# Performance work log

Hardware: AMD Instinct MI355X
Metric: run time of the kernel (lower is better)

The kernel has to match this reference:

```python
import jax, jax.numpy as jnp
import numpy as np

N, L, D = 4096, 16, 768        # nodes, max name tokens, gpt2 embed dim
NH_NAME = 4                    # name-encoder attention heads
H, NH, NL, C = 1024, 8, 4, 16  # hidden, encoder heads, encoder layers, classes
XF = 256                       # raw node feature dim; feat_dim = XF + D = 1024
VOCAB = 50257


def _ln(x, g, b, eps=1e-5):
    m = jnp.mean(x, axis=-1, keepdims=True)
    v = jnp.var(x, axis=-1, keepdims=True)
    return (x - m) * jax.lax.rsqrt(v + eps) * g + b


def _mha(x, in_w, in_b, out_w, out_b, nh, key_mask=None):
    # x: [B, S, E]; in_w: [3E, E] (torch nn.MultiheadAttention packed qkv)
    B, S, E = x.shape
    dh = E // nh
    qkv = x @ in_w.T + in_b
    q, k, v = jnp.split(qkv, 3, axis=-1)
    q = q.reshape(B, S, nh, dh)
    k = k.reshape(B, S, nh, dh)
    v = v.reshape(B, S, nh, dh)
    scores = jnp.einsum('bqhd,bkhd->bhqk', q, k) / jnp.sqrt(jnp.asarray(dh, x.dtype))
    if key_mask is not None:
        scores = jnp.where(key_mask[:, None, None, :], scores, jnp.asarray(-1e9, x.dtype))
    a = jax.nn.softmax(scores, axis=-1)
    o = jnp.einsum('bhqk,bkhd->bqhd', a, v).reshape(B, S, E)
    return o @ out_w.T + out_b


def setup_inputs() -> dict:
    key = jax.random.key(0)
    ks = jax.random.split(key, 16)
    s = 0.02
    r = lambda i, shape: jax.random.normal(ks[i], shape, jnp.float32) * s
    return {
        'name_tokens': jax.random.randint(ks[0], (N, L), 0, VOCAB),
        'name_lens': jax.random.randint(ks[1], (N,), 1, L + 1),
        'x_feats': jax.random.normal(ks[2], (N, XF), jnp.float32),
        'wte': r(3, (VOCAB, D)),
        'mha_in_w': r(4, (3 * D, D)), 'mha_in_b': jnp.zeros((3 * D,), jnp.float32),
        'mha_out_w': r(5, (D, D)), 'mha_out_b': jnp.zeros((D,), jnp.float32),
        'bott_w': r(6, (H, XF + D)), 'bott_b': jnp.zeros((H,), jnp.float32),
        'enc_in_w': r(7, (NL, 3 * H, H)), 'enc_in_b': jnp.zeros((NL, 3 * H), jnp.float32),
        'enc_out_w': r(8, (NL, H, H)), 'enc_out_b': jnp.zeros((NL, H), jnp.float32),
        'enc_ln1_g': jnp.ones((NL, H), jnp.float32), 'enc_ln1_b': jnp.zeros((NL, H), jnp.float32),
        'enc_ln2_g': jnp.ones((NL, H), jnp.float32), 'enc_ln2_b': jnp.zeros((NL, H), jnp.float32),
        'enc_ff1_w': r(9, (NL, 2 * H, H)), 'enc_ff1_b': jnp.zeros((NL, 2 * H), jnp.float32),
        'enc_ff2_w': r(10, (NL, H, 2 * H)), 'enc_ff2_b': jnp.zeros((NL, H), jnp.float32),
        'cls_w': r(11, (C, H)), 'cls_b': jnp.zeros((C,), jnp.float32),
    }


def reference(name_tokens, name_lens, x_feats, wte,
              mha_in_w, mha_in_b, mha_out_w, mha_out_b,
              bott_w, bott_b,
              enc_in_w, enc_in_b, enc_out_w, enc_out_b,
              enc_ln1_g, enc_ln1_b, enc_ln2_g, enc_ln2_b,
              enc_ff1_w, enc_ff1_b, enc_ff2_w, enc_ff2_b,
              cls_w, cls_b):
    # --- GraphNameEncoder: batched over all N ragged name sequences ---
    mask = jnp.arange(L)[None, :] < name_lens[:, None]          # [N, L] valid-token mask
    emb = wte[name_tokens]                                      # [N, L, D]
    attn = _mha(emb, mha_in_w, mha_in_b, mha_out_w, mha_out_b, NH_NAME, key_mask=mask)
    name_emb = jnp.sum(jnp.where(mask[:, :, None], attn, 0.0), axis=1)  # [N, D]
    x = jnp.concatenate([x_feats, name_emb], axis=-1)           # [N, XF + D]
    # --- bottleneck ---
    x = x @ bott_w.T + bott_b                                   # [N, H]
    # --- TransformerEncoder on seq_len=1 (x.unsqueeze(1)), post-norm, relu ---
    h = x[:, None, :]                                           # [N, 1, H]
    for l in range(NL):
        a = _mha(h, enc_in_w[l], enc_in_b[l], enc_out_w[l], enc_out_b[l], NH)
        h = _ln(h + a, enc_ln1_g[l], enc_ln1_b[l])
        f = jax.nn.relu(h @ enc_ff1_w[l].T + enc_ff1_b[l]) @ enc_ff2_w[l].T + enc_ff2_b[l]
        h = _ln(h + f, enc_ln2_g[l], enc_ln2_b[l])
    out = h @ cls_w.T + cls_b                                   # [N, 1, C]
    return out[:, 0, :]                                         # squeeze -> [N, C]
```

## Files before the change

### kernel.cpp

```cpp
#include <hip/hip_runtime.h>

typedef unsigned short bf16_t;
typedef __attribute__((ext_vector_type(8))) __bf16 bf16x8;
typedef __attribute__((ext_vector_type(4))) float f32x4;

__device__ __forceinline__ float bf2f(unsigned v) { return __uint_as_float(v << 16); }
__device__ __forceinline__ bf16_t f2bf(float f) {
  unsigned u = __float_as_uint(f);
  return (bf16_t)((u + 0x7fffu + ((u >> 16) & 1u)) >> 16);
}
__device__ __forceinline__ unsigned pack2(float a, float b) {
  return (unsigned)f2bf(a) | ((unsigned)f2bf(b) << 16);
}

__global__ __launch_bounds__(256) void scan_lens(const int* __restrict__ lens,
                                                 int* __restrict__ offs,
                                                 int* __restrict__ Mact) {
  __shared__ int wsum[4];
  const int t = threadIdx.x;
  int v[16]; int s = 0;
#pragma unroll
  for (int i = 0; i < 16; i++) { v[i] = lens[t * 16 + i]; s += v[i]; }
  const int lane = t & 63, w = t >> 6;
  int x = s;
#pragma unroll
  for (int o = 1; o < 64; o <<= 1) {
    int y = __shfl_up(x, o);
    if (lane >= o) x += y;
  }
  if (lane == 63) wsum[w] = x;
  __syncthreads();
  int base = 0;
  for (int i = 0; i < w; i++) base += wsum[i];
  int run = base + x - s;
#pragma unroll
  for (int i = 0; i < 16; i++) { offs[t * 16 + i] = run; run += v[i]; }
  if (t == 255) Mact[0] = run;
}

__global__ void cvt_f32_bf16(const float* __restrict__ src, bf16_t* __restrict__ dst, long n4) {
  long i = (long)blockIdx.x * blockDim.x + threadIdx.x;
  if (i >= n4) return;
  float4 v = ((const float4*)src)[i];
  ((uint2*)dst)[i] = make_uint2(pack2(v.x, v.y), pack2(v.z, v.w));
}

__global__ __launch_bounds__(256) void cvt_trans(const float* __restrict__ src,
                                                 bf16_t* __restrict__ dst) {
  __shared__ float tile[32][33];
  const int l = blockIdx.z;
  const int bx = blockIdx.x * 32;
  const int by = blockIdx.y * 32;
  const float* s = src + (size_t)l * 3 * 1024 * 1024 + 2 * 1024 * 1024;
  const int tx = threadIdx.x & 31, ty = threadIdx.x >> 5;
#pragma unroll
  for (int i = 0; i < 32; i += 8)
    tile[ty + i][tx] = s[(size_t)(by + ty + i) * 1024 + bx + tx];
  __syncthreads();
  bf16_t* d = dst + (size_t)l * 1024 * 1024;
#pragma unroll
  for (int i = 0; i < 32; i += 8)
    d[(size_t)(bx + ty + i) * 1024 + by + tx] = f2bf(tile[tx][ty + i]);
}

__global__ __launch_bounds__(256) void bias_comb(const float* __restrict__ enc_out_w,
                                                 const float* __restrict__ enc_in_b,
                                                 const float* __restrict__ enc_out_b,
                                                 float* __restrict__ bc) {
  const int l = blockIdx.y;
  const int wave = threadIdx.x >> 6, lane = threadIdx.x & 63;
  const float* w = enc_out_w + (size_t)l * 1024 * 1024;
  const float* bv = enc_in_b + (size_t)l * 3072 + 2048;
  for (int c = wave; c < 16; c += 4) {
    int i = blockIdx.x * 16 + c;
    const float* wr = w + (size_t)i * 1024;
    float acc = 0.f;
    for (int j = lane; j < 1024; j += 64) acc += wr[j] * bv[j];
#pragma unroll
    for (int o = 32; o > 0; o >>= 1) acc += __shfl_down(acc, o);
    if (lane == 0) bc[(size_t)l * 1024 + i] = acc + enc_out_b[(size_t)l * 1024 + i];
  }
}

__global__ void gather_emb_c(const int* __restrict__ tok, const int* __restrict__ lens,
                             const int* __restrict__ offs, const float* __restrict__ wte,
                             bf16_t* __restrict__ emb) {
  long i = (long)blockIdx.x * blockDim.x + threadIdx.x;
  if (i >= 65536L * 192L) return;
  long nl = i / 192; int cg = (int)(i % 192);
  int n = (int)(nl >> 4), l = (int)(nl & 15);
  if (l >= lens[n]) return;
  long ro = (long)offs[n] + l;
  int t = tok[nl];
  float4 v = *(const float4*)(wte + (long)t * 768 + cg * 4);
  ((uint2*)emb)[ro * 192 + cg] = make_uint2(pack2(v.x, v.y), pack2(v.z, v.w));
}

__global__ void xfeat_lenf(const float* __restrict__ xf, const int* __restrict__ lens,
                           bf16_t* __restrict__ x, float* __restrict__ lenf) {
  long i = (long)blockIdx.x * blockDim.x + threadIdx.x;
  if (i < 4096) lenf[i] = (float)lens[i];
  if (i >= 4096L * 64L) return;
  int row = (int)(i >> 6); int c4 = (int)(i & 63) * 4;
  float4 v = *(const float4*)(xf + (long)row * 256 + c4);
  *(uint2*)(x + (long)row * 1024 + c4) = make_uint2(pack2(v.x, v.y), pack2(v.z, v.w));
}

#define BM 128
#define BN 128
#define BK 32
#define SBT (BM * BK + BN * BK)

__device__ __forceinline__ void async16(const void* g, void* l) {
  __builtin_amdgcn_global_load_lds((const __attribute__((address_space(1))) void*)g,
                                   (__attribute__((address_space(3))) void*)l, 16, 0, 0);
}

__global__ __launch_bounds__(256, 2) void gemm_bt(
    const bf16_t* __restrict__ A, const bf16_t* __restrict__ W,
    const float* __restrict__ bias, bf16_t* __restrict__ C,
    int K, int ldc, const int* __restrict__ Mp,
    long sA, long sB, long sC) {
  const int m0 = blockIdx.y * BM;
  if (Mp != nullptr && m0 >= *Mp) return;
  __shared__ __attribute__((aligned(16))) bf16_t smem[2 * SBT];
  const int t = threadIdx.x;
  const int n0 = blockIdx.x * BN;
  const int z = blockIdx.z;
  const int lane = t & 63;
  const int wr = t >> 7;
  const int wc = (t >> 6) & 1;
  const int quad = lane >> 4;
  const int r16 = lane & 15;

  f32x4 acc[4][4] = {};

  const int c0 = t, c1 = t + 256;
  const int row0 = c0 >> 2, kp0 = (c0 & 3) << 3;
  const int row1 = c1 >> 2, kp1 = (c1 & 3) << 3;
  const size_t oc0 = (size_t)(c0 & ~63) * 8;
  const size_t oc1 = (size_t)(c1 & ~63) * 8;
  const bf16_t* Ab = A + (size_t)z * sA + (size_t)m0 * K;
  const bf16_t* Wb = W + (size_t)z * sB + (size_t)n0 * K;
  bf16_t* Cb = C + (size_t)z * sC;

  auto stage = [&](int b, int k0) {
    bf16_t* As = smem + (size_t)b * SBT;
    bf16_t* Bs = As + BM * BK;
    async16(Ab + (size_t)row0 * K + k0 + kp0, As + oc0);
    async16(Ab + (size_t)row1 * K + k0 + kp1, As + oc1);
    async16(Wb + (size_t)row0 * K + k0 + kp0, Bs + oc0);
    async16(Wb + (size_t)row1 * K + k0 + kp1, Bs + oc1);
  };

  stage(0, 0);
  __syncthreads();
  int cur = 0;
  for (int k0 = 0; k0 < K; k0 += BK) {
    if (k0 + BK < K) stage(cur ^ 1, k0 + BK);
    const bf16_t* As = smem + (size_t)cur * SBT;
    const bf16_t* Bs = As + BM * BK;
    bf16x8 af[4], bfr[4];
#pragma unroll
    for (int i = 0; i < 4; i++) {
      af[i]  = *(const bf16x8*)(As + (wr * 64 + i * 16 + r16) * BK + quad * 8);
      bfr[i] = *(const bf16x8*)(Bs + (wc * 64 + i * 16 + r16) * BK + quad * 8);
    }
#pragma unroll
    for (int i = 0; i < 4; i++)
#pragma unroll
      for (int j = 0; j < 4; j++)
        acc[i][j] = __builtin_amdgcn_mfma_f32_16x16x32_bf16(af[i], bfr[j], acc[i][j], 0, 0, 0);
    __syncthreads();
    cur ^= 1;
  }

  const int ldcs = 136;
  bf16_t* Cs = smem;
#pragma unroll
  for (int s = 0; s < 4; s++) {
    if (wr == (s >> 1)) {
      const int ib = (s & 1) * 2;
#pragma unroll
      for (int i2 = 0; i2 < 2; i2++) {
        const int i = ib + i2;
#pragma unroll
        for (int j = 0; j < 4; j++) {
          int col = wc * 64 + j * 16 + r16;
          float bv = bias ? bias[n0 + col] : 0.0f;
#pragma unroll
          for (int r = 0; r < 4; r++)
            Cs[(i2 * 16 + quad * 4 + r) * ldcs + col] = f2bf(acc[i][j][r] + bv);
        }
      }
    }
    __syncthreads();
    {
      const int rl = t >> 4, cl = (t & 15) * 8;
#pragma unroll
      for (int p = 0; p < 2; p++) {
        int row = rl + p * 16;
        bf16x8 v = *(const bf16x8*)(Cs + row * ldcs + cl);
        *(bf16x8*)(Cb + (size_t)(m0 + s * 32 + row) * ldc + n0 + cl) = v;
      }
    }
    __syncthreads();
  }
}

#define S64 (128 * 64 + 64 * 64)

template <bool RELU>
__global__ __launch_bounds__(256, 3) void gemm128x64(
    const bf16_t* __restrict__ A, const bf16_t* __restrict__ W,
    const float* __restrict__ bias, const float* __restrict__ rowscale,
    bf16_t* __restrict__ C, int K, int ldc) {
  __shared__ __attribute__((aligned(16))) bf16_t smem[2 * S64];
  const int t = threadIdx.x;
  const int m0 = blockIdx.x * 128, n0 = blockIdx.y * 64;
  const int lane = t & 63, w = t >> 6;
  const int quad = lane >> 4, r16 = lane & 15;
  f32x4 acc[2][4] = {};
  int rowA[4], kpA[4];
  size_t oA[4];
#pragma unroll
  for (int i = 0; i < 4; i++) {
    int c = t + i * 256;
    rowA[i] = c >> 3;
    kpA[i] = ((c & 7) ^ (rowA[i] & 7)) << 3;
    oA[i] = (size_t)(c & ~63) * 8;
  }
  int rowB[2], kpB[2];
  size_t oB[2];
#pragma unroll
  for (int i = 0; i < 2; i++) {
    int c = t + i * 256;
    rowB[i] = c >> 3;
    kpB[i] = ((c & 7) ^ (rowB[i] & 7)) << 3;
    oB[i] = (size_t)(c & ~63) * 8;
  }
  const bf16_t* Ab = A + (size_t)m0 * K;
  const bf16_t* Wb = W + (size_t)n0 * K;

  auto stage = [&](int b, int k0) {
    bf16_t* As = smem + (size_t)b * S64;
    bf16_t* Bs = As + 128 * 64;
#pragma unroll
    for (int i = 0; i < 4; i++) async16(Ab + (size_t)rowA[i] * K + k0 + kpA[i], As + oA[i]);
#pragma unroll
    for (int i = 0; i < 2; i++) async16(Wb + (size_t)rowB[i] * K + k0 + kpB[i], Bs + oB[i]);
  };

  stage(0, 0);
  __syncthreads();
  int cur = 0;
  for (int k0 = 0; k0 < K; k0 += 64) {
    if (k0 + 64 < K) stage(cur ^ 1, k0 + 64);
    const bf16_t* As = smem + (size_t)cur * S64;
    const bf16_t* Bs = As + 128 * 64;
#pragma unroll
    for (int kk8 = 0; kk8 < 8; kk8 += 4) {
      bf16x8 af[2], bfr[4];
#pragma unroll
      for (int i = 0; i < 2; i++) {
        int Ra = w * 32 + i * 16 + r16;
        af[i] = *(const bf16x8*)(As + Ra * 64 + (((kk8 + quad) ^ (Ra & 7)) << 3));
      }
#pragma unroll
      for (int j = 0; j < 4; j++) {
        int Rb = j * 16 + r16;
        bfr[j] = *(const bf16x8*)(Bs + Rb * 64 + (((kk8 + quad) ^ (Rb & 7)) << 3));
      }
#pragma unroll
      for (int i = 0; i < 2; i++)
#pragma unroll
        for (int j = 0; j < 4; j++)
          acc[i][j] = __builtin_amdgcn_mfma_f32_16x16x32_bf16(af[i], bfr[j], acc[i][j], 0, 0, 0);
    }
    __syncthreads();
    cur ^= 1;
  }

  const int ldcs = 72;
  bf16_t* Cs = smem;
#pragma unroll
  for (int i = 0; i < 2; i++) {
#pragma unroll
    for (int j = 0; j < 4; j++) {
      int col = j * 16 + r16;
      float bv = bias ? bias[n0 + col] : 0.0f;
#pragma unroll
      for (int r = 0; r < 4; r++) {
        int row = w * 32 + i * 16 + quad * 4 + r;
        float sc = rowscale ? rowscale[m0 + row] : 1.0f;
        float v = acc[i][j][r] + bv * sc;
        if (RELU) v = fmaxf(v, 0.0f);
        Cs[row * ldcs + col] = f2bf(v);
      }
    }
  }
  __syncthreads();
  {
    const int rl = t >> 3, cl = (t & 7) * 8;
#pragma unroll
    for (int p = 0; p < 4; p++) {
      int row = rl + p * 32;
      bf16x8 v = *(const bf16x8*)(Cs + row * ldcs + cl);
      *(bf16x8*)(C + (size_t)(m0 + row) * ldc + n0 + cl) = v;
    }
  }
}

__global__ __launch_bounds__(64) void attn_name(const bf16_t* __restrict__ qkv,
                                                const int* __restrict__ lens,
                                                const int* __restrict__ offs,
                                                bf16_t* __restrict__ s) {
  const int n = blockIdx.x, h = blockIdx.y;
  const int lane = threadIdx.x;
  __shared__ unsigned short qs[16][208];
  __shared__ unsigned short ks[16][208];
  __shared__ unsigned short vs[16][208];
  __shared__ float ps[16][16];
  __shared__ float wj[16];
  const int len = lens[n];
  const bf16_t* base = qkv + (size_t)offs[n] * 2304 + h * 192;
  for (int g = lane; g < len * 48; g += 64) {
    int row = g / 48, c4 = (g % 48) * 4;
    const bf16_t* p = base + (size_t)row * 2304 + c4;
    uint2 a;
    a = *(const uint2*)p;
    *(unsigned*)&qs[row][c4] = a.x; *(unsigned*)&qs[row][c4 + 2] = a.y;
    a = *(const uint2*)(p + 768);
    *(unsigned*)&ks[row][c4] = a.x; *(unsigned*)&ks[row][c4 + 2] = a.y;
    a = *(const uint2*)(p + 1536);
    *(unsigned*)&vs[row][c4] = a.x; *(unsigned*)&vs[row][c4 + 2] = a.y;
  }
  __syncthreads();
  {
    const int l = lane >> 2, j0 = (lane & 3) * 4;
    float s0 = 0, s1 = 0, s2 = 0, s3 = 0;
    for (int d = 0; d < 192; d++) {
      float q = bf2f(qs[l][d]);
      s0 += q * bf2f(ks[j0 + 0][d]);
      s1 += q * bf2f(ks[j0 + 1][d]);
      s2 += q * bf2f(ks[j0 + 2][d]);
      s3 += q * bf2f(ks[j0 + 3][d]);
    }
    const float sc = 0.07216878f;
    ps[l][j0 + 0] = s0 * sc; ps[l][j0 + 1] = s1 * sc;
    ps[l][j0 + 2] = s2 * sc; ps[l][j0 + 3] = s3 * sc;
  }
  __syncthreads();
  if (lane < 16) {
    float m = -1e30f;
    for (int j = 0; j < len; j++) m = fmaxf(m, ps[lane][j]);
    float sum = 0.f;
    for (int j = 0; j < len; j++) sum += __expf(ps[lane][j] - m);
    float inv = 1.0f / sum;
    for (int j = 0; j < 16; j++) ps[lane][j] = (j < len) ? __expf(ps[lane][j] - m) * inv : 0.0f;
  }
  __syncthreads();
  if (lane < 16) {
    float a = 0.f;
    for (int l2 = 0; l2 < len; l2++) a += ps[l2][lane];
    wj[lane] = a;
  }
  __syncthreads();
  for (int d = lane; d < 192; d += 64) {
    float a = 0.f;
    for (int j = 0; j < len; j++) a += wj[j] * bf2f(vs[j][d]);
    s[(size_t)n * 768 + h * 192 + d] = f2bf(a);
  }
}

__global__ __launch_bounds__(256) void ln_res(bf16_t* __restrict__ h, const bf16_t* __restrict__ d,
                                              const float* __restrict__ g, const float* __restrict__ b) {
  const int n = blockIdx.x, t = threadIdx.x;
  __shared__ float s1[4], s2[4];
  bf16_t* hr = h + (size_t)n * 1024;
  const bf16_t* dr = d + (size_t)n * 1024;
  float x[4];
  float sum = 0.f, ss = 0.f;
#pragma unroll
  for (int i = 0; i < 4; i++) {
    int c = t + i * 256;
    float v = bf2f(hr[c]) + bf2f(dr[c]);
    x[i] = v; sum += v; ss += v * v;
  }
#pragma unroll
  for (int o = 32; o > 0; o >>= 1) { sum += __shfl_down(sum, o); ss += __shfl_down(ss, o); }
  if ((t & 63) == 0) { s1[t >> 6] = sum; s2[t >> 6] = ss; }
  __syncthreads();
  sum = s1[0] + s1[1] + s1[2] + s1[3];
  ss  = s2[0] + s2[1] + s2[2] + s2[3];
  const float mean = sum * (1.0f / 1024.0f);
  const float var = ss * (1.0f / 1024.0f) - mean * mean;
  const float rstd = rsqrtf(var + 1e-5f);
#pragma unroll
  for (int i = 0; i < 4; i++) {
    int c = t + i * 256;
    hr[c] = f2bf((x[i] - mean) * rstd * g[c] + b[c]);
  }
}

__global__ __launch_bounds__(256) void cls_head(const bf16_t* __restrict__ h,
                                                const float* __restrict__ cw,
                                                const float* __restrict__ cb,
                                                float* __restrict__ out) {
  const int n = blockIdx.x, t = threadIdx.x, wave = t >> 6, lane = t & 63;
  const bf16_t* hr = h + (size_t)n * 1024;
  for (int c = wave; c < 16; c += 4) {
    const float* wr = cw + c * 1024;
    float acc = 0.f;
    for (int i = lane; i < 1024; i += 64) acc += bf2f(hr[i]) * wr[i];
#pragma unroll
    for (int o = 32; o > 0; o >>= 1) acc += __shfl_down(acc, o);
    if (lane == 0) out[(size_t)n * 16 + c] = acc + cb[c];
  }
}

extern "C" void kernel_launch(void* const* d_in, const int* in_sizes, int n_in,
                              void* d_out, int out_size, void* d_ws, size_t ws_size,
                              hipStream_t stream) {
  (void)in_sizes; (void)n_in; (void)out_size; (void)ws_size;
  const int* name_tokens = (const int*)d_in[0];
  const int* name_lens   = (const int*)d_in[1];
  const float* x_feats   = (const float*)d_in[2];
  const float* wte       = (const float*)d_in[3];
  const float* mha_in_w  = (const float*)d_in[4];
  const float* mha_in_b  = (const float*)d_in[5];
  const float* mha_out_w = (const float*)d_in[6];
  const float* mha_out_b = (const float*)d_in[7];
  const float* bott_w    = (const float*)d_in[8];
  const float* bott_b    = (const float*)d_in[9];
  const float* enc_in_w  = (const float*)d_in[10];
  const float* enc_in_b  = (const float*)d_in[11];
  const float* enc_out_w = (const float*)d_in[12];
  const float* enc_out_b = (const float*)d_in[13];
  const float* enc_ln1_g = (const float*)d_in[14];
  const float* enc_ln1_b = (const float*)d_in[15];
  const float* enc_ln2_g = (const float*)d_in[16];
  const float* enc_ln2_b = (const float*)d_in[17];
  const float* enc_ff1_w = (const float*)d_in[18];
  const float* enc_ff1_b = (const float*)d_in[19];
  const float* enc_ff2_w = (const float*)d_in[20];
  const float* enc_ff2_b = (const float*)d_in[21];
  const float* cls_w     = (const float*)d_in[22];
  const float* cls_b     = (const float*)d_in[23];
  float* out = (float*)d_out;

  char* base = (char*)d_ws;
  size_t off = 0;
  auto alloc = [&](size_t bytes) -> char* {
    char* p = base + off;
    off = (off + bytes + 255) & ~(size_t)255;
    return p;
  };
  bf16_t* w_qkv  = (bf16_t*)alloc((size_t)2304 * 768 * 2);
  bf16_t* w_out  = (bf16_t*)alloc((size_t)768 * 768 * 2);
  bf16_t* w_bott = (bf16_t*)alloc((size_t)1024 * 1024 * 2);
  bf16_t* w_vT   = (bf16_t*)alloc((size_t)4 * 1024 * 1024 * 2);
  bf16_t* w_enco = (bf16_t*)alloc((size_t)4 * 1024 * 1024 * 2);
  bf16_t* w_ff1  = (bf16_t*)alloc((size_t)4 * 2048 * 1024 * 2);
  bf16_t* w_ff2  = (bf16_t*)alloc((size_t)4 * 1024 * 2048 * 2);
  float*  lenf   = (float*)alloc((size_t)4096 * 4);
  int*    offs   = (int*)alloc((size_t)4096 * 4);
  int*    Mact   = (int*)alloc((size_t)256);
  char* reuse = alloc((size_t)65536 * 768 * 2);
  bf16_t* emb = (bf16_t*)reuse;
  bf16_t* s_  = (bf16_t*)reuse;
  bf16_t* x_  = (bf16_t*)(reuse + 6291456);
  bf16_t* h_  = (bf16_t*)(reuse + 6291456 + 8388608);
  bf16_t* v_  = (bf16_t*)(reuse + 6291456 + 2 * 8388608);
  bf16_t* a_  = (bf16_t*)(reuse + 6291456 + 3 * 8388608);
  bf16_t* f1_ = (bf16_t*)(reuse + 6291456 + 4 * 8388608);
  bf16_t* qkv = (bf16_t*)alloc((size_t)65536 * 2304 * 2);
  bf16_t* wc = (bf16_t*)qkv;
  float*  bc = (float*)((char*)qkv + (size_t)4 * 1024 * 1024 * 2);

  dim3 b256(256);
  auto g1 = [](long n4) { return dim3((unsigned)((n4 + 255) / 256)); };

  scan_lens<<<dim3(1), b256, 0, stream>>>(name_lens, offs, Mact);

  cvt_f32_bf16<<<g1(442368), b256, 0, stream>>>(mha_in_w, w_qkv, 442368L);
  cvt_f32_bf16<<<g1(147456), b256, 0, stream>>>(mha_out_w, w_out, 147456L);
  cvt_f32_bf16<<<g1(262144), b256, 0, stream>>>(bott_w, w_bott, 262144L);
  cvt_trans<<<dim3(32, 32, 4), b256, 0, stream>>>(enc_in_w, w_vT);
  cvt_f32_bf16<<<g1(1048576), b256, 0, stream>>>(enc_out_w, w_enco, 1048576L);
  cvt_f32_bf16<<<g1(2097152), b256, 0, stream>>>(enc_ff1_w, w_ff1, 2097152L);
  cvt_f32_bf16<<<g1(2097152), b256, 0, stream>>>(enc_ff2_w, w_ff2, 2097152L);

  gather_emb_c<<<dim3(49152), b256, 0, stream>>>(name_tokens, name_lens, offs, wte, emb);
  gemm_bt<<<dim3(18, 512), b256, 0, stream>>>(emb, w_qkv, mha_in_b, qkv, 768, 2304, Mact,
                                              0L, 0L, 0L);
  xfeat_lenf<<<dim3(1024), b256, 0, stream>>>(x_feats, name_lens, x_, lenf);
  attn_name<<<dim3(4096, 4), dim3(64), 0, stream>>>(qkv, name_lens, offs, s_);

  gemm_bt<<<dim3(8, 8, 4), b256, 0, stream>>>(
      w_enco, w_vT, (const float*)nullptr, wc, 1024, 1024, (const int*)nullptr,
      (long)1024 * 1024, (long)1024 * 1024, (long)1024 * 1024);
  bias_comb<<<dim3(64, 4), b256, 0, stream>>>(enc_out_w, enc_in_b, enc_out_b, bc);

  gemm128x64<false><<<dim3(32, 12), b256, 0, stream>>>(s_, w_out, mha_out_b, lenf,
                                                       x_ + 256, 768, 1024);
  gemm128x64<false><<<dim3(32, 16), b256, 0, stream>>>(x_, w_bott, bott_b,
                                                       (const float*)nullptr, h_, 1024, 1024);
  for (int l = 0; l < 4; l++) {
    gemm128x64<false><<<dim3(32, 16), b256, 0, stream>>>(
        h_, wc + (size_t)l * 1024 * 1024, bc + (size_t)l * 1024,
        (const float*)nullptr, a_, 1024, 1024);
    ln_res<<<dim3(4096), b256, 0, stream>>>(h_, a_, enc_ln1_g + l * 1024, enc_ln1_b + l * 1024);
    gemm128x64<true><<<dim3(32, 32), b256, 0, stream>>>(
        h_, w_ff1 + (size_t)l * 2048 * 1024, enc_ff1_b + l * 2048,
        (const float*)nullptr, f1_, 1024, 2048);
    gemm128x64<false><<<dim3(32, 16), b256, 0, stream>>>(
        f1_, w_ff2 + (size_t)l * 1024 * 2048, enc_ff2_b + l * 1024,
        (const float*)nullptr, v_, 2048, 1024);
    ln_res<<<dim3(4096), b256, 0, stream>>>(h_, v_, enc_ln2_g + l * 1024, enc_ln2_b + l * 1024);
  }
  cls_head<<<dim3(4096), b256, 0, stream>>>(h_, cls_w, cls_b, out);
}
```

Measured before the change: 1.213 ms.

## Add XCD-aware tile swizzle, LDS XOR swizzle, and halve gemm128x64 K-step

Introduces an XCD-aware block-index remap so that consecutive M-tiles land on the same XCD for better L2 reuse. Grids are transposed so blockIdx.x indexes N tiles. gemm_bt gets an XOR swizzle on its 32-wide LDS rows to cut bank conflicts, and its launch bound rises to 4 blocks per CU. gemm128x64 moves from BK=64 to BK=32 with a smaller LDS footprint and an occupancy target of 6 blocks, trading more loop iterations and barriers for more resident waves. The FF1 launch keeps dim3(32,32), so its meaning changes under the remap but it still covers the full output.

```diff
diff --git a/kernel.cpp b/kernel.cpp
--- a/kernel.cpp
+++ b/kernel.cpp
@@ -11,6 +11,20 @@
 }
 __device__ __forceinline__ unsigned pack2(float a, float b) {
   return (unsigned)f2bf(a) | ((unsigned)f2bf(b) << 16);
+}
+
+__device__ __forceinline__ void swz_decode(int& mt, int& nt) {
+  const int NT = gridDim.x, MT = gridDim.y;
+  int lin = blockIdx.y * NT + blockIdx.x;
+  if ((MT & 7) == 0 && gridDim.z == 1) {
+    int xcd = lin & 7;
+    int j = lin >> 3;
+    mt = (j / NT) * 8 + xcd;
+    nt = j % NT;
+  } else {
+    mt = blockIdx.y;
+    nt = blockIdx.x;
+  }
 }
 
 __global__ __launch_bounds__(256) void scan_lens(const int* __restrict__ lens,
@@ -116,16 +130,20 @@
                                    (__attribute__((address_space(3))) void*)l, 16, 0, 0);
 }
 
-__global__ __launch_bounds__(256, 2) void gemm_bt(
+__device__ __forceinline__ int swz4(int row) { return (row & 3) ^ ((row >> 2) & 3); }
+
+__global__ __launch_bounds__(256, 4) void gemm_bt(
     const bf16_t* __restrict__ A, const bf16_t* __restrict__ W,
     const float* __restrict__ bias, bf16_t* __restrict__ C,
     int K, int ldc, const int* __restrict__ Mp,
     long sA, long sB, long sC) {
-  const int m0 = blockIdx.y * BM;
+  int mt, nt;
+  swz_decode(mt, nt);
+  const int m0 = mt * BM;
   if (Mp != nullptr && m0 >= *Mp) return;
   __shared__ __attribute__((aligned(16))) bf16_t smem[2 * SBT];
   const int t = threadIdx.x;
-  const int n0 = blockIdx.x * BN;
+  const int n0 = nt * BN;
   const int z = blockIdx.z;
   const int lane = t & 63;
   const int wr = t >> 7;
@@ -136,8 +154,8 @@
   f32x4 acc[4][4] = {};
 
   const int c0 = t, c1 = t + 256;
-  const int row0 = c0 >> 2, kp0 = (c0 & 3) << 3;
-  const int row1 = c1 >> 2, kp1 = (c1 & 3) << 3;
+  const int row0 = c0 >> 2, kp0 = ((c0 & 3) ^ swz4(row0)) << 3;
+  const int row1 = c1 >> 2, kp1 = ((c1 & 3) ^ swz4(row1)) << 3;
   const size_t oc0 = (size_t)(c0 & ~63) * 8;
   const size_t oc1 = (size_t)(c1 & ~63) * 8;
   const bf16_t* Ab = A + (size_t)z * sA + (size_t)m0 * K;
@@ -163,8 +181,10 @@
     bf16x8 af[4], bfr[4];
 #pragma unroll
     for (int i = 0; i < 4; i++) {
-      af[i]  = *(const bf16x8*)(As + (wr * 64 + i * 16 + r16) * BK + quad * 8);
-      bfr[i] = *(const bf16x8*)(Bs + (wc * 64 + i * 16 + r16) * BK + quad * 8);
+      int Ra = wr * 64 + i * 16 + r16;
+      af[i]  = *(const bf16x8*)(As + Ra * BK + ((quad ^ swz4(Ra)) << 3));
+      int Rb = wc * 64 + i * 16 + r16;
+      bfr[i] = *(const bf16x8*)(Bs + Rb * BK + ((quad ^ swz4(Rb)) << 3));
     }
 #pragma unroll
     for (int i = 0; i < 4; i++)
@@ -208,75 +228,67 @@
   }
 }
 
-#define S64 (128 * 64 + 64 * 64)
+#define S64 (128 * 32 + 64 * 32)
 
 template <bool RELU>
-__global__ __launch_bounds__(256, 3) void gemm128x64(
+__global__ __launch_bounds__(256, 6) void gemm128x64(
     const bf16_t* __restrict__ A, const bf16_t* __restrict__ W,
     const float* __restrict__ bias, const float* __restrict__ rowscale,
     bf16_t* __restrict__ C, int K, int ldc) {
   __shared__ __attribute__((aligned(16))) bf16_t smem[2 * S64];
   const int t = threadIdx.x;
-  const int m0 = blockIdx.x * 128, n0 = blockIdx.y * 64;
+  int mt, nt;
+  swz_decode(mt, nt);
+  const int m0 = mt * 128, n0 = nt * 64;
   const int lane = t & 63, w = t >> 6;
   const int quad = lane >> 4, r16 = lane & 15;
   f32x4 acc[2][4] = {};
-  int rowA[4], kpA[4];
-  size_t oA[4];
-#pragma unroll
-  for (int i = 0; i < 4; i++) {
-    int c = t + i * 256;
-    rowA[i] = c >> 3;
-    kpA[i] = ((c & 7) ^ (rowA[i] & 7)) << 3;
-    oA[i] = (size_t)(c & ~63) * 8;
-  }
-  int rowB[2], kpB[2];
-  size_t oB[2];
+  int rowA[2], kpA[2];
+  size_t oA[2];
 #pragma unroll
   for (int i = 0; i < 2; i++) {
     int c = t + i * 256;
-    rowB[i] = c >> 3;
-    kpB[i] = ((c & 7) ^ (rowB[i] & 7)) << 3;
-    oB[i] = (size_t)(c & ~63) * 8;
-  }
+    rowA[i] = c >> 2;
+    kpA[i] = ((c & 3) ^ swz4(rowA[i])) << 3;
+    oA[i] = (size_t)(c & ~63) * 8;
+  }
+  const int rowB = t >> 2;
+  const int kpB = ((t & 3) ^ swz4(rowB)) << 3;
+  const size_t oB = (size_t)(t & ~63) * 8;
   const bf16_t* Ab = A + (size_t)m0 * K;
   const bf16_t* Wb = W + (size_t)n0 * K;
 
   auto stage = [&](int b, int k0) {
     bf16_t* As = smem + (size_t)b * S64;
-    bf16_t* Bs = As + 128 * 64;
-#pragma unroll
-    for (int i = 0; i < 4; i++) async16(Ab + (size_t)rowA[i] * K + k0 + kpA[i], As + oA[i]);
-#pragma unroll
-    for (int i = 0; i < 2; i++) async16(Wb + (size_t)rowB[i] * K + k0 + kpB[i], Bs + oB[i]);
+    bf16_t* Bs = As + 128 * 32;
+    async16(Ab + (size_t)rowA[0] * K + k0 + kpA[0], As + oA[0]);
+    async16(Ab + (size_t)rowA[1] * K + k0 + kpA[1], As + oA[1]);
+    async16(Wb + (size_t)rowB * K + k0 + kpB, Bs + oB);
   };
 
   stage(0, 0);
   __syncthreads();
   int cur = 0;
-  for (int k0 = 0; k0 < K; k0 += 64) {
-    if (k0 + 64 < K) stage(cur ^ 1, k0 + 64);
+  for (int k0 = 0; k0 < K; k0 += 32) {
+    if (k0 + 32 < K) stage(cur ^ 1, k0 + 32);
     const bf16_t* As = smem + (size_t)cur * S64;
-    const bf16_t* Bs = As + 128 * 64;
-#pragma unroll
-    for (int kk8 = 0; kk8 < 8; kk8 += 4) {
-      bf16x8 af[2], bfr[4];
-#pragma unroll
-      for (int i = 0; i < 2; i++) {
-        int Ra = w * 32 + i * 16 + r16;
-        af[i] = *(const bf16x8*)(As + Ra * 64 + (((kk8 + quad) ^ (Ra & 7)) << 3));
-      }
-#pragma unroll
-      for (int j = 0; j < 4; j++) {
-        int Rb = j * 16 + r16;
-        bfr[j] = *(const bf16x8*)(Bs + Rb * 64 + (((kk8 + quad) ^ (Rb & 7)) << 3));
-      }
-#pragma unroll
-      for (int i = 0; i < 2; i++)
-#pragma unroll
-        for (int j = 0; j < 4; j++)
-          acc[i][j] = __builtin_amdgcn_mfma_f32_16x16x32_bf16(af[i], bfr[j], acc[i][j], 0, 0, 0);
-    }
+    const bf16_t* Bs = As + 128 * 32;
+    bf16x8 af[2], bfr[4];
+#pragma unroll
+    for (int i = 0; i < 2; i++) {
+      int Ra = w * 32 + i * 16 + r16;
+      af[i] = *(const bf16x8*)(As + Ra * 32 + ((quad ^ swz4(Ra)) << 3));
+    }
+#pragma unroll
+    for (int j = 0; j < 4; j++) {
+      int Rb = j * 16 + r16;
+      bfr[j] = *(const bf16x8*)(Bs + Rb * 32 + ((quad ^ swz4(Rb)) << 3));
+    }
+#pragma unroll
+    for (int i = 0; i < 2; i++)
+#pragma unroll
+      for (int j = 0; j < 4; j++)
+        acc[i][j] = __builtin_amdgcn_mfma_f32_16x16x32_bf16(af[i], bfr[j], acc[i][j], 0, 0, 0);
     __syncthreads();
     cur ^= 1;
   }
@@ -502,19 +514,19 @@
       (long)1024 * 1024, (long)1024 * 1024, (long)1024 * 1024);
   bias_comb<<<dim3(64, 4), b256, 0, stream>>>(enc_out_w, enc_in_b, enc_out_b, bc);
 
-  gemm128x64<false><<<dim3(32, 12), b256, 0, stream>>>(s_, w_out, mha_out_b, lenf,
+  gemm128x64<false><<<dim3(12, 32), b256, 0, stream>>>(s_, w_out, mha_out_b, lenf,
                                                        x_ + 256, 768, 1024);
-  gemm128x64<false><<<dim3(32, 16), b256, 0, stream>>>(x_, w_bott, bott_b,
+  gemm128x64<false><<<dim3(16, 32), b256, 0, stream>>>(x_, w_bott, bott_b,
                                                        (const float*)nullptr, h_, 1024, 1024);
   for (int l = 0; l < 4; l++) {
-    gemm128x64<false><<<dim3(32, 16), b256, 0, stream>>>(
+    gemm128x64<false><<<dim3(16, 32), b256, 0, stream>>>(
         h_, wc + (size_t)l * 1024 * 1024, bc + (size_t)l * 1024,
         (const float*)nullptr, a_, 1024, 1024);
     ln_res<<<dim3(4096), b256, 0, stream>>>(h_, a_, enc_ln1_g + l * 1024, enc_ln1_b + l * 1024);
     gemm128x64<true><<<dim3(32, 32), b256, 0, stream>>>(
         h_, w_ff1 + (size_t)l * 2048 * 1024, enc_ff1_b + l * 2048,
         (const float*)nullptr, f1_, 1024, 2048);
-    gemm128x64<false><<<dim3(32, 16), b256, 0, stream>>>(
+    gemm128x64<false><<<dim3(16, 32), b256, 0, stream>>>(
         f1_, w_ff2 + (size_t)l * 1024 * 2048, enc_ff2_b + l * 1024,
         (const float*)nullptr, v_, 2048, 1024);
     ln_res<<<dim3(4096), b256, 0, stream>>>(h_, v_, enc_ln2_g + l * 1024, enc_ln2_b + l * 1024);
```

New measurement: 1.229 ms. About the same (+1.3%).

## Rewrite name attention with MFMA scores and single-buffer the 128x64 GEMM

Applied to the files above, without the earlier changes.

The name-attention kernel now runs one 256-thread block per node, one wavefront per head. QK^T is computed with bf16 MFMA instructions straight from global memory, and softmax and the column sums use wavefront shuffles instead of shared-memory scalar loops. This is meant to cut the heavy scalar dot-product and synchronisation cost of the old per-head kernel. Separately, the 128x64 GEMM drops its double-buffered async LDS pipeline for a single buffer and raises its occupancy hint from 3 to 4. That trades load/compute overlap for more resident blocks.

```diff
diff --git a/kernel.cpp b/kernel.cpp
--- a/kernel.cpp
+++ b/kernel.cpp
@@ -106,15 +106,15 @@
   *(uint2*)(x + (long)row * 1024 + c4) = make_uint2(pack2(v.x, v.y), pack2(v.z, v.w));
 }
 
+__device__ __forceinline__ void async16(const void* g, void* l) {
+  __builtin_amdgcn_global_load_lds((const __attribute__((address_space(1))) void*)g,
+                                   (__attribute__((address_space(3))) void*)l, 16, 0, 0);
+}
+
 #define BM 128
 #define BN 128
 #define BK 32
 #define SBT (BM * BK + BN * BK)
-
-__device__ __forceinline__ void async16(const void* g, void* l) {
-  __builtin_amdgcn_global_load_lds((const __attribute__((address_space(1))) void*)g,
-                                   (__attribute__((address_space(3))) void*)l, 16, 0, 0);
-}
 
 __global__ __launch_bounds__(256, 2) void gemm_bt(
     const bf16_t* __restrict__ A, const bf16_t* __restrict__ W,
@@ -208,56 +208,47 @@
   }
 }
 
-#define S64 (128 * 64 + 64 * 64)
-
 template <bool RELU>
-__global__ __launch_bounds__(256, 3) void gemm128x64(
+__global__ __launch_bounds__(256, 4) void gemm128x64(
     const bf16_t* __restrict__ A, const bf16_t* __restrict__ W,
     const float* __restrict__ bias, const float* __restrict__ rowscale,
     bf16_t* __restrict__ C, int K, int ldc) {
-  __shared__ __attribute__((aligned(16))) bf16_t smem[2 * S64];
+  __shared__ __attribute__((aligned(16))) bf16_t smem[128 * 64 + 64 * 64];
+  bf16_t* As = smem;
+  bf16_t* Bs = smem + 128 * 64;
   const int t = threadIdx.x;
   const int m0 = blockIdx.x * 128, n0 = blockIdx.y * 64;
   const int lane = t & 63, w = t >> 6;
   const int quad = lane >> 4, r16 = lane & 15;
   f32x4 acc[2][4] = {};
   int rowA[4], kpA[4];
-  size_t oA[4];
+  bf16_t* lA[4];
 #pragma unroll
   for (int i = 0; i < 4; i++) {
     int c = t + i * 256;
     rowA[i] = c >> 3;
     kpA[i] = ((c & 7) ^ (rowA[i] & 7)) << 3;
-    oA[i] = (size_t)(c & ~63) * 8;
+    lA[i] = As + (size_t)(c & ~63) * 8;
   }
   int rowB[2], kpB[2];
-  size_t oB[2];
+  bf16_t* lB[2];
 #pragma unroll
   for (int i = 0; i < 2; i++) {
     int c = t + i * 256;
     rowB[i] = c >> 3;
     kpB[i] = ((c & 7) ^ (rowB[i] & 7)) << 3;
-    oB[i] = (size_t)(c & ~63) * 8;
+    lB[i] = Bs + (size_t)(c & ~63) * 8;
   }
   const bf16_t* Ab = A + (size_t)m0 * K;
   const bf16_t* Wb = W + (size_t)n0 * K;
 
-  auto stage = [&](int b, int k0) {
-    bf16_t* As = smem + (size_t)b * S64;
-    bf16_t* Bs = As + 128 * 64;
-#pragma unroll
-    for (int i = 0; i < 4; i++) async16(Ab + (size_t)rowA[i] * K + k0 + kpA[i], As + oA[i]);
-#pragma unroll
-    for (int i = 0; i < 2; i++) async16(Wb + (size_t)rowB[i] * K + k0 + kpB[i], Bs + oB[i]);
-  };
-
-  stage(0, 0);
-  __syncthreads();
-  int cur = 0;
   for (int k0 = 0; k0 < K; k0 += 64) {
-    if (k0 + 64 < K) stage(cur ^ 1, k0 + 64);
-    const bf16_t* As = smem + (size_t)cur * S64;
-    const bf16_t* Bs = As + 128 * 64;
+    __syncthreads();
+#pragma unroll
+    for (int i = 0; i < 4; i++) async16(Ab + (size_t)rowA[i] * K + k0 + kpA[i], lA[i]);
+#pragma unroll
+    for (int i = 0; i < 2; i++) async16(Wb + (size_t)rowB[i] * K + k0 + kpB[i], lB[i]);
+    __syncthreads();
 #pragma unroll
     for (int kk8 = 0; kk8 < 8; kk8 += 4) {
       bf16x8 af[2], bfr[4];
@@ -277,10 +268,9 @@
         for (int j = 0; j < 4; j++)
           acc[i][j] = __builtin_amdgcn_mfma_f32_16x16x32_bf16(af[i], bfr[j], acc[i][j], 0, 0, 0);
     }
-    __syncthreads();
-    cur ^= 1;
-  }
-
+  }
+
+  __syncthreads();
   const int ldcs = 72;
   bf16_t* Cs = smem;
 #pragma unroll
@@ -311,66 +301,79 @@
   }
 }
 
-__global__ __launch_bounds__(64) void attn_name(const bf16_t* __restrict__ qkv,
-                                                const int* __restrict__ lens,
-                                                const int* __restrict__ offs,
-                                                bf16_t* __restrict__ s) {
-  const int n = blockIdx.x, h = blockIdx.y;
-  const int lane = threadIdx.x;
-  __shared__ unsigned short qs[16][208];
-  __shared__ unsigned short ks[16][208];
-  __shared__ unsigned short vs[16][208];
-  __shared__ float ps[16][16];
-  __shared__ float wj[16];
+__global__ __launch_bounds__(256) void attn_name(const bf16_t* __restrict__ qkv,
+                                                 const int* __restrict__ lens,
+                                                 const int* __restrict__ offs,
+                                                 bf16_t* __restrict__ s) {
+  const int n = blockIdx.x;
+  const int h = threadIdx.x >> 6;
+  const int lane = threadIdx.x & 63;
+  const int quad = lane >> 4, r16 = lane & 15;
+  __shared__ bf16_t vs[4][16][200];
+  __shared__ float wjs[4][16];
   const int len = lens[n];
-  const bf16_t* base = qkv + (size_t)offs[n] * 2304 + h * 192;
-  for (int g = lane; g < len * 48; g += 64) {
-    int row = g / 48, c4 = (g % 48) * 4;
-    const bf16_t* p = base + (size_t)row * 2304 + c4;
-    uint2 a;
-    a = *(const uint2*)p;
-    *(unsigned*)&qs[row][c4] = a.x; *(unsigned*)&qs[row][c4 + 2] = a.y;
-    a = *(const uint2*)(p + 768);
-    *(unsigned*)&ks[row][c4] = a.x; *(unsigned*)&ks[row][c4 + 2] = a.y;
-    a = *(const uint2*)(p + 1536);
-    *(unsigned*)&vs[row][c4] = a.x; *(unsigned*)&vs[row][c4 + 2] = a.y;
-  }
-  __syncthreads();
-  {
-    const int l = lane >> 2, j0 = (lane & 3) * 4;
-    float s0 = 0, s1 = 0, s2 = 0, s3 = 0;
-    for (int d = 0; d < 192; d++) {
-      float q = bf2f(qs[l][d]);
-      s0 += q * bf2f(ks[j0 + 0][d]);
-      s1 += q * bf2f(ks[j0 + 1][d]);
-      s2 += q * bf2f(ks[j0 + 2][d]);
-      s3 += q * bf2f(ks[j0 + 3][d]);
-    }
-    const float sc = 0.07216878f;
-    ps[l][j0 + 0] = s0 * sc; ps[l][j0 + 1] = s1 * sc;
-    ps[l][j0 + 2] = s2 * sc; ps[l][j0 + 3] = s3 * sc;
-  }
-  __syncthreads();
-  if (lane < 16) {
-    float m = -1e30f;
-    for (int j = 0; j < len; j++) m = fmaxf(m, ps[lane][j]);
-    float sum = 0.f;
-    for (int j = 0; j < len; j++) sum += __expf(ps[lane][j] - m);
-    float inv = 1.0f / sum;
-    for (int j = 0; j < 16; j++) ps[lane][j] = (j < len) ? __expf(ps[lane][j] - m) * inv : 0.0f;
-  }
-  __syncthreads();
-  if (lane < 16) {
-    float a = 0.f;
-    for (int l2 = 0; l2 < len; l2++) a += ps[l2][lane];
-    wj[lane] = a;
-  }
-  __syncthreads();
-  for (int d = lane; d < 192; d += 64) {
-    float a = 0.f;
-    for (int j = 0; j < len; j++) a += wj[j] * bf2f(vs[j][d]);
-    s[(size_t)n * 768 + h * 192 + d] = f2bf(a);
-  }
+  const size_t rbase = (size_t)offs[n] * 2304 + h * 192;
+  const bf16_t* qp = qkv + rbase;
+  const bf16_t* kp = qkv + rbase + 768;
+  const bf16_t* vp = qkv + rbase + 1536;
+
+  const int vrow = lane >> 2, vc = lane & 3;
+  const int vrr = (vrow < len) ? vrow : 0;
+  uint2 vbuf[12];
+#pragma unroll
+  for (int i = 0; i < 12; i++)
+    vbuf[i] = *(const uint2*)(vp + (size_t)vrr * 2304 + (vc + i * 4) * 4);
+
+  const int rr = (r16 < len) ? r16 : 0;
+  f32x4 acc = {};
+#pragma unroll
+  for (int ks = 0; ks < 6; ks++) {
+    bf16x8 aq = *(const bf16x8*)(qp + (size_t)rr * 2304 + ks * 32 + quad * 8);
+    bf16x8 bk = *(const bf16x8*)(kp + (size_t)rr * 2304 + ks * 32 + quad * 8);
+    acc = __builtin_amdgcn_mfma_f32_16x16x32_bf16(aq, bk, acc, 0, 0, 0);
+  }
+
+  const float sc = 0.07216878f;
+  float p[4];
+#pragma unroll
+  for (int r = 0; r < 4; r++) {
+    float x = (r16 < len) ? acc[r] * sc : -1e30f;
+    float m = x;
+    m = fmaxf(m, __shfl_xor(m, 1));
+    m = fmaxf(m, __shfl_xor(m, 2));
+    m = fmaxf(m, __shfl_xor(m, 4));
+    m = fmaxf(m, __shfl_xor(m, 8));
+    float e = __expf(x - m);
+    float sum = e;
+    sum += __shfl_xor(sum, 1);
+    sum += __shfl_xor(sum, 2);
+    sum += __shfl_xor(sum, 4);
+    sum += __shfl_xor(sum, 8);
+    p[r] = ((quad * 4 + r) < len) ? e / sum : 0.0f;
+  }
+  float wj = p[0] + p[1] + p[2] + p[3];
+  wj += __shfl_xor(wj, 16);
+  wj += __shfl_xor(wj, 32);
+  if (quad == 0) wjs[h][r16] = wj;
+
+  if (vrow < len) {
+#pragma unroll
+    for (int i = 0; i < 12; i++)
+      *(uint2*)&vs[h][vrow][(vc + i * 4) * 4] = vbuf[i];
+  }
+  __syncthreads();
+
+  float o0 = 0.f, o1 = 0.f, o2 = 0.f;
+  for (int j = 0; j < len; j++) {
+    float w = wjs[h][j];
+    o0 += w * bf2f(vs[h][j][lane]);
+    o1 += w * bf2f(vs[h][j][lane + 64]);
+    o2 += w * bf2f(vs[h][j][lane + 128]);
+  }
+  bf16_t* op = s + (size_t)n * 768 + h * 192;
+  op[lane] = f2bf(o0);
+  op[lane + 64] = f2bf(o1);
+  op[lane + 128] = f2bf(o2);
 }
 
 __global__ __launch_bounds__(256) void ln_res(bf16_t* __restrict__ h, const bf16_t* __restrict__ d,
@@ -495,7 +498,7 @@
   gemm_bt<<<dim3(18, 512), b256, 0, stream>>>(emb, w_qkv, mha_in_b, qkv, 768, 2304, Mact,
                                               0L, 0L, 0L);
   xfeat_lenf<<<dim3(1024), b256, 0, stream>>>(x_feats, name_lens, x_, lenf);
-  attn_name<<<dim3(4096, 4), dim3(64), 0, stream>>>(qkv, name_lens, offs, s_);
+  attn_name<<<dim3(4096), b256, 0, stream>>>(qkv, name_lens, offs, s_);
 
   gemm_bt<<<dim3(8, 8, 4), b256, 0, stream>>>(
       w_enco, w_vT, (const float*)nullptr, wc, 1024, 1024, (const int*)nullptr,
```

New measurement: 1.097 ms. 9.5% less time.
